# Kernel tuning notes

Measured on AMD Instinct MI355X. Metric: run time of the kernel, lower is better.

The kernel has to match this reference:

```python
import jax, jax.numpy as jnp
import numpy as np

TEMP_UPDATE = 1e-05
EPS = 1e-12  # torch F.normalize eps


def _l2norm(x, axis):
    n = jnp.sqrt(jnp.sum(x * x, axis=axis, keepdims=True))
    return x / jnp.maximum(n, EPS)


def setup_inputs() -> dict:
    key = jax.random.key(0)
    k1, k2 = jax.random.split(key)
    query = jax.random.normal(k1, (64, 256, 512), dtype=jnp.float32)
    keys = jax.random.normal(k2, (2048, 512), dtype=jnp.float32)
    return {"query": query, "keys": keys}


def reference(query, keys):
    bs, t, d = query.shape
    m = keys.shape[0]
    # F.normalize(query, dim=2)
    q = _l2norm(query, axis=2)
    qr = q.reshape(bs * t, d)                      # [N, d]
    score = qr @ keys.T                            # [N, m]
    score_query = jax.nn.softmax(score, axis=0)    # softmax over queries per slot
    score_memory = jax.nn.softmax(score, axis=1)   # softmax over slots per query
    # topk(1) over memory dim -> argmax slot per query
    g = jnp.argmax(score_memory, axis=1)           # [N] int
    col_max = jnp.max(score_query, axis=0)         # [m]
    # weight per query: score_query[n, g_n] / max(score_query[:, g_n])
    w = jnp.take_along_axis(score_query, g[:, None], axis=1)[:, 0] / col_max[g]
    # fused scatter-add replacing the per-slot python loop
    query_update = jax.ops.segment_sum(w[:, None] * qr, g, num_segments=m)  # [m, d]
    updated = _l2norm(TEMP_UPDATE * query_update + keys, axis=1)
    return jax.lax.stop_gradient(updated)  # original returns .detach()
```

## Files before the change

kernel.cpp:

```cpp
#include <hip/hip_runtime.h>
#include <math.h>

#define N_Q     16384
#define DDIM    512
#define M_SLOTS 2048
#define EPSN    1e-12f
#define TEMPU   1e-5f
#define KSCALE  25.4f
#define QSCALE  127.0f
#define INV_S   (1.0f / (127.0f * 25.4f))
#define NZBLK   73
#define BCAP    32

typedef unsigned int u32;
typedef unsigned long long u64;
typedef __attribute__((ext_vector_type(4))) int i32x4;

__device__ __forceinline__ void gld_lds16(const void* g, void* l) {
    __builtin_amdgcn_global_load_lds(
        (const __attribute__((address_space(1))) u32*)(g),
        (__attribute__((address_space(3))) u32*)(l), 16, 0, 0);
}
__device__ __forceinline__ float block_reduce_sum_128(float v, float* sred, int t) {
    #pragma unroll
    for (int o = 32; o > 0; o >>= 1) v += __shfl_down(v, o, 64);
    if ((t & 63) == 0) sred[t >> 6] = v;
    __syncthreads();
    return sred[0] + sred[1];
}
__device__ __forceinline__ char q8(float x, float s) {
    int v = __float2int_rn(x * s);
    v = v < -127 ? -127 : (v > 127 ? 127 : v);
    return (char)v;
}

__global__ __launch_bounds__(128) void k_prep(const float* __restrict__ q,
                                              const float* __restrict__ keys,
                                              char* __restrict__ qi8,
                                              char* __restrict__ ki8,
                                              float4* __restrict__ zbase) {
    __shared__ float sred[2];
    int b = blockIdx.x;
    int t = threadIdx.x;
    if (b < N_Q) {
        float4 v = ((const float4*)(q + (size_t)b * DDIM))[t];
        float ss = v.x * v.x + v.y * v.y + v.z * v.z + v.w * v.w;
        ss = block_reduce_sum_128(ss, sred, t);
        float s = QSCALE / fmaxf(sqrtf(ss), EPSN);
        char4 o;
        o.x = q8(v.x, s);
        o.y = q8(v.y, s);
        o.z = q8(v.z, s);
        o.w = q8(v.w, s);
        ((char4*)(qi8 + (size_t)b * DDIM))[t] = o;
    } else if (b < N_Q + M_SLOTS) {
        int r = b - N_Q;
        float4 v = ((const float4*)(keys + (size_t)r * DDIM))[t];
        char4 o;
        o.x = q8(v.x, KSCALE);
        o.y = q8(v.y, KSCALE);
        o.z = q8(v.z, KSCALE);
        o.w = q8(v.w, KSCALE);
        ((char4*)(ki8 + (size_t)r * DDIM))[t] = o;
    } else {
        int idx = (b - (N_Q + M_SLOTS)) * 128 + t;
        zbase[idx] = make_float4(0.f, 0.f, 0.f, 0.f);
    }
}

__global__ __launch_bounds__(256) void k_score(const char* __restrict__ qi8,
                                               const char* __restrict__ ki8,
                                               u64* __restrict__ rowpack,
                                               u32* __restrict__ colmax) {
    __shared__ char sA[3][128 * 64];
    __shared__ char sB[3][128 * 64];

    int t = threadIdx.x;
    int lane = t & 63;
    int wid = t >> 6;
    int wrow = wid >> 1;
    int wcol = wid & 1;
    int lr = lane & 15;
    int kc = lane >> 4;

    int n0 = blockIdx.y * 128;
    int j0 = blockIdx.x * 128;

    int srow = t >> 2;
    int scolB = (t & 3) * 16;

    const char* gA0 = qi8 + (size_t)(n0 + srow) * DDIM + scolB;
    const char* gA1 = qi8 + (size_t)(n0 + 64 + srow) * DDIM + scolB;
    const char* gB0 = ki8 + (size_t)(j0 + srow) * DDIM + scolB;
    const char* gB1 = ki8 + (size_t)(j0 + 64 + srow) * DDIM + scolB;

    i32x4 acc[4][4] = {};

#define STAGE(buf, k0)  do {                                   \
        gld_lds16(gA0 + (k0), &sA[buf][t * 16]);               \
        gld_lds16(gA1 + (k0), &sA[buf][4096 + t * 16]);        \
        gld_lds16(gB0 + (k0), &sB[buf][t * 16]);               \
        gld_lds16(gB1 + (k0), &sB[buf][4096 + t * 16]);        \
    } while (0)

    STAGE(0, 0);
    STAGE(1, 64);
    asm volatile("s_waitcnt vmcnt(4)" ::: "memory");
    __builtin_amdgcn_s_barrier();
    __builtin_amdgcn_sched_barrier(0);

    #pragma unroll
    for (int kt = 0; kt < 8; ++kt) {
        const int cur = kt % 3;
        if (kt < 6) STAGE((kt + 2) % 3, (kt + 2) * 64);

        i32x4 a[4], b[4];
        #pragma unroll
        for (int i = 0; i < 4; ++i)
            a[i] = *(const i32x4*)&sA[cur][(wrow * 64 + i * 16 + lr) * 64 + kc * 16];
        #pragma unroll
        for (int j = 0; j < 4; ++j)
            b[j] = *(const i32x4*)&sB[cur][(wcol * 64 + j * 16 + lr) * 64 + kc * 16];
        #pragma unroll
        for (int i = 0; i < 4; ++i)
            #pragma unroll
            for (int j = 0; j < 4; ++j)
                acc[i][j] = __builtin_amdgcn_mfma_i32_16x16x64_i8(a[i], b[j], acc[i][j], 0, 0, 0);

        if (kt < 6)       asm volatile("s_waitcnt vmcnt(4)" ::: "memory");
        else if (kt == 6) asm volatile("s_waitcnt vmcnt(0)" ::: "memory");
        if (kt < 7) {
            __builtin_amdgcn_s_barrier();
            __builtin_amdgcn_sched_barrier(0);
        }
    }
#undef STAGE

    #pragma unroll
    for (int i = 0; i < 4; ++i) {
        #pragma unroll
        for (int r = 0; r < 4; ++r) {
            int v = acc[i][0][r];
            int c = j0 + wcol * 64 + lr;
            #pragma unroll
            for (int j = 1; j < 4; ++j) {
                int vj = acc[i][j][r];
                int cj = j0 + wcol * 64 + j * 16 + lr;
                if (vj > v) { v = vj; c = cj; }
            }
            #pragma unroll
            for (int off = 1; off < 16; off <<= 1) {
                int ov = __shfl_xor(v, off, 64);
                int oc = __shfl_xor(c, off, 64);
                if (ov > v || (ov == v && oc < c)) { v = ov; c = oc; }
            }
            if (lr == 0) {
                int grow = n0 + wrow * 64 + i * 16 + kc * 4 + r;
                u64 pk = ((u64)(u32)(v ^ 0x80000000) << 32) | (u64)(~(u32)c);
                atomicMax(rowpack + grow, pk);
            }
        }
    }
    #pragma unroll
    for (int j = 0; j < 4; ++j) {
        int m = acc[0][j][0];
        #pragma unroll
        for (int i = 0; i < 4; ++i)
            #pragma unroll
            for (int r = 0; r < 4; ++r) m = max(m, acc[i][j][r]);
        m = max(m, __shfl_xor(m, 16, 64));
        m = max(m, __shfl_xor(m, 32, 64));
        if (kc == 0) atomicMax(colmax + j0 + wcol * 64 + j * 16 + lr,
                               (u32)m ^ 0x80000000u);
    }
}

__global__ __launch_bounds__(256) void k_fill(const u64* __restrict__ rowpack,
                                              const u32* __restrict__ colmax,
                                              u32* __restrict__ cur,
                                              u32* __restrict__ bperm,
                                              float* __restrict__ bw,
                                              u32* __restrict__ ovf_cnt,
                                              u32* __restrict__ ovf_n,
                                              float* __restrict__ ovf_w) {
    int n = blockIdx.x * 256 + threadIdx.x;
    u64 p = rowpack[n];
    int vi = (int)(((u32)(p >> 32)) ^ 0x80000000u);
    int g = (int)(~(u32)(p & 0xFFFFFFFFull));
    int cm = (int)(colmax[g] ^ 0x80000000u);
    float w = expf((float)(vi - cm) * INV_S);
    u32 pos = atomicAdd(cur + g, 1u);
    if (pos < BCAP) {
        bperm[g * BCAP + pos] = (u32)n;
        bw[g * BCAP + pos] = w;
    } else {
        u32 o = atomicAdd(ovf_cnt, 1u);
        ovf_n[o] = ((u32)g << 16) | (u32)n;
        ovf_w[o] = w;
    }
}

__global__ __launch_bounds__(128) void k_gather_final(const char* __restrict__ qi8,
                                                      const u32* __restrict__ cur,
                                                      const u32* __restrict__ bperm,
                                                      const float* __restrict__ bw,
                                                      const u32* __restrict__ ovf_cnt,
                                                      const u32* __restrict__ ovf_n,
                                                      const float* __restrict__ ovf_w,
                                                      const float* __restrict__ keys,
                                                      float* __restrict__ out) {
    __shared__ float sred[2];
    int j = blockIdx.x;
    int t = threadIdx.x;
    u32 c = cur[j];
    u32 cnt = c < BCAP ? c : BCAP;
    float ax = 0.f, ay = 0.f, az = 0.f, aw = 0.f;
    for (u32 i = 0; i < cnt; ++i) {
        u32 n = bperm[j * BCAP + i];
        float wq = bw[j * BCAP + i] * (1.0f / 127.0f);
        char4 q4 = ((const char4*)(qi8 + (size_t)n * DDIM))[t];
        ax = fmaf(wq, (float)q4.x, ax);
        ay = fmaf(wq, (float)q4.y, ay);
        az = fmaf(wq, (float)q4.z, az);
        aw = fmaf(wq, (float)q4.w, aw);
    }
    if (c > BCAP) {
        u32 oc = *ovf_cnt;
        for (u32 i = 0; i < oc; ++i) {
            u32 e = ovf_n[i];
            if ((e >> 16) == (u32)j) {
                u32 n = e & 0xFFFFu;
                float wq = ovf_w[i] * (1.0f / 127.0f);
                char4 q4 = ((const char4*)(qi8 + (size_t)n * DDIM))[t];
                ax = fmaf(wq, (float)q4.x, ax);
                ay = fmaf(wq, (float)q4.y, ay);
                az = fmaf(wq, (float)q4.z, az);
                aw = fmaf(wq, (float)q4.w, aw);
            }
        }
    }
    float4 k4 = ((const float4*)(keys + (size_t)j * DDIM))[t];
    float4 v;
    v.x = fmaf(TEMPU, ax, k4.x);
    v.y = fmaf(TEMPU, ay, k4.y);
    v.z = fmaf(TEMPU, az, k4.z);
    v.w = fmaf(TEMPU, aw, k4.w);
    float ss = v.x * v.x + v.y * v.y + v.z * v.z + v.w * v.w;
    ss = block_reduce_sum_128(ss, sred, t);
    float inv = 1.0f / fmaxf(sqrtf(ss), EPSN);
    v.x *= inv; v.y *= inv; v.z *= inv; v.w *= inv;
    ((float4*)(out + (size_t)j * DDIM))[t] = v;
}

extern "C" void kernel_launch(void* const* d_in, const int* in_sizes, int n_in,
                              void* d_out, int out_size, void* d_ws, size_t ws_size,
                              hipStream_t stream) {
    const float* query = (const float*)d_in[0];
    const float* keys  = (const float*)d_in[1];
    float* out = (float*)d_out;

    char* ws = (char*)d_ws;
    const size_t OFF_QI8   = 0;
    const size_t OFF_ROW   = 8388608;
    const size_t OFF_CMAX  = OFF_ROW + 131072;
    const size_t OFF_CUR   = OFF_CMAX + 8192;
    const size_t OFF_OVFC  = OFF_CUR + 8192;
    const size_t OFF_BPERM = OFF_OVFC + 2048;
    const size_t OFF_BW    = OFF_BPERM + 262144;
    const size_t OFF_OVFN  = OFF_BW + 262144;
    const size_t OFF_OVFW  = OFF_OVFN + 65536;
    const size_t OFF_KI8   = OFF_OVFW + 65536;

    char*   qi8    = ws + OFF_QI8;
    u64*    rowpack= (u64*)(ws + OFF_ROW);
    u32*    cmax   = (u32*)(ws + OFF_CMAX);
    u32*    cur    = (u32*)(ws + OFF_CUR);
    u32*    ovfc   = (u32*)(ws + OFF_OVFC);
    u32*    bperm  = (u32*)(ws + OFF_BPERM);
    float*  bw     = (float*)(ws + OFF_BW);
    u32*    ovfn   = (u32*)(ws + OFF_OVFN);
    float*  ovfw   = (float*)(ws + OFF_OVFW);
    char*   ki8    = ws + OFF_KI8;

    k_prep<<<N_Q + M_SLOTS + NZBLK, 128, 0, stream>>>(query, keys, qi8, ki8,
                                                      (float4*)(ws + OFF_ROW));

    dim3 g2(M_SLOTS / 128, N_Q / 128);
    k_score<<<g2, 256, 0, stream>>>(qi8, ki8, rowpack, cmax);

    k_fill<<<N_Q / 256, 256, 0, stream>>>(rowpack, cmax, cur, bperm, bw,
                                          ovfc, ovfn, ovfw);
    k_gather_final<<<M_SLOTS, 128, 0, stream>>>(qi8, cur, bperm, bw,
                                                ovfc, ovfn, ovfw, keys, out);
}
```

Before: 72.19 us.

## Make score GEMM persistent with cross-tile prefetch of next tile's K stages

Converts the int8 score GEMM from one block per 128x128 tile (2048 blocks) into a persistent grid of 768 blocks that stride over tiles. The triple-buffered global-to-LDS pipeline now continues across tile boundaries, so the first two K stages of the next tile load while the current tile's last stages compute and its argmax/colmax epilogue runs. This targets per-block launch and pipeline ramp-up cost, in exchange for uneven tile counts per block (2048/768 is not integral, so some blocks do 3 tiles and others 2) and more complex buffer indexing.

New measurement: 89.42 us. +23.9%, slower.

```diff
diff --git a/kernel.cpp b/kernel.cpp
--- a/kernel.cpp
+++ b/kernel.cpp
@@ -11,6 +11,7 @@
 #define INV_S   (1.0f / (127.0f * 25.4f))
 #define NZBLK   73
 #define BCAP    32
+#define PBLK    768
 
 typedef unsigned int u32;
 typedef unsigned long long u64;
@@ -83,96 +84,129 @@
     int lr = lane & 15;
     int kc = lane >> 4;
 
-    int n0 = blockIdx.y * 128;
-    int j0 = blockIdx.x * 128;
-
     int srow = t >> 2;
     int scolB = (t & 3) * 16;
 
-    const char* gA0 = qi8 + (size_t)(n0 + srow) * DDIM + scolB;
-    const char* gA1 = qi8 + (size_t)(n0 + 64 + srow) * DDIM + scolB;
-    const char* gB0 = ki8 + (size_t)(j0 + srow) * DDIM + scolB;
-    const char* gB1 = ki8 + (size_t)(j0 + 64 + srow) * DDIM + scolB;
+    int bid = blockIdx.x;
+    int nt = (2048 - bid + PBLK - 1) / PBLK;
+    int total = nt * 8;
+
+#define TILE_PTRS(tile, pA, pB)  do {                                  \
+        int n0_ = ((tile) >> 4) * 128;                                 \
+        int j0_ = ((tile) & 15) * 128;                                 \
+        pA = qi8 + (size_t)(n0_ + srow) * DDIM + scolB;                \
+        pB = ki8 + (size_t)(j0_ + srow) * DDIM + scolB;                \
+    } while (0)
+
+#define STAGE4(buf, pA, pB, koff)  do {                                \
+        gld_lds16((pA) + (koff),              &sA[buf][t * 16]);       \
+        gld_lds16((pA) + 64 * DDIM + (koff),  &sA[buf][4096 + t * 16]);\
+        gld_lds16((pB) + (koff),              &sB[buf][t * 16]);       \
+        gld_lds16((pB) + 64 * DDIM + (koff),  &sB[buf][4096 + t * 16]);\
+    } while (0)
 
     i32x4 acc[4][4] = {};
 
-#define STAGE(buf, k0)  do {                                   \
-        gld_lds16(gA0 + (k0), &sA[buf][t * 16]);               \
-        gld_lds16(gA1 + (k0), &sA[buf][4096 + t * 16]);        \
-        gld_lds16(gB0 + (k0), &sB[buf][t * 16]);               \
-        gld_lds16(gB1 + (k0), &sB[buf][4096 + t * 16]);        \
-    } while (0)
-
-    STAGE(0, 0);
-    STAGE(1, 64);
+    {
+        const char *pA, *pB;
+        TILE_PTRS(bid, pA, pB);
+        STAGE4(0, pA, pB, 0);
+        STAGE4(1, pA, pB, 64);
+    }
     asm volatile("s_waitcnt vmcnt(4)" ::: "memory");
     __builtin_amdgcn_s_barrier();
     __builtin_amdgcn_sched_barrier(0);
 
-    #pragma unroll
-    for (int kt = 0; kt < 8; ++kt) {
-        const int cur = kt % 3;
-        if (kt < 6) STAGE((kt + 2) % 3, (kt + 2) * 64);
-
-        i32x4 a[4], b[4];
+    int b0 = 0;
+    #pragma unroll 1
+    for (int tt = 0; tt < nt; ++tt) {
+        int tileC = bid + tt * PBLK;
+        int n0 = (tileC >> 4) * 128;
+        int j0 = (tileC & 15) * 128;
+        int tileN = (tt + 1 < nt) ? tileC + PBLK : tileC;
+        const char *cA, *cB, *nA, *nB;
+        TILE_PTRS(tileC, cA, cB);
+        TILE_PTRS(tileN, nA, nB);
+        int bufs[3] = { b0, (b0 + 1) % 3, (b0 + 2) % 3 };
+
         #pragma unroll
-        for (int i = 0; i < 4; ++i)
-            a[i] = *(const i32x4*)&sA[cur][(wrow * 64 + i * 16 + lr) * 64 + kc * 16];
+        for (int kt = 0; kt < 8; ++kt) {
+            int vs = tt * 8 + kt;
+            if (vs + 2 < total) {
+                int sbuf = bufs[(kt + 2) % 3];
+                if (kt < 6) STAGE4(sbuf, cA, cB, (kt + 2) * 64);
+                else        STAGE4(sbuf, nA, nB, (kt - 6) * 64);
+            }
+            {
+                int cbuf = bufs[kt % 3];
+                i32x4 a[4], b[4];
+                #pragma unroll
+                for (int i = 0; i < 4; ++i)
+                    a[i] = *(const i32x4*)&sA[cbuf][(wrow * 64 + i * 16 + lr) * 64 + kc * 16];
+                #pragma unroll
+                for (int j = 0; j < 4; ++j)
+                    b[j] = *(const i32x4*)&sB[cbuf][(wcol * 64 + j * 16 + lr) * 64 + kc * 16];
+                #pragma unroll
+                for (int i = 0; i < 4; ++i)
+                    #pragma unroll
+                    for (int j = 0; j < 4; ++j)
+                        acc[i][j] = __builtin_amdgcn_mfma_i32_16x16x64_i8(a[i], b[j], acc[i][j], 0, 0, 0);
+            }
+            if (vs + 2 < total)       asm volatile("s_waitcnt vmcnt(4)" ::: "memory");
+            else if (vs == total - 2) asm volatile("s_waitcnt vmcnt(0)" ::: "memory");
+            if (vs < total - 1) {
+                __builtin_amdgcn_s_barrier();
+                __builtin_amdgcn_sched_barrier(0);
+            }
+        }
+
         #pragma unroll
-        for (int j = 0; j < 4; ++j)
-            b[j] = *(const i32x4*)&sB[cur][(wcol * 64 + j * 16 + lr) * 64 + kc * 16];
+        for (int i = 0; i < 4; ++i) {
+            #pragma unroll
+            for (int r = 0; r < 4; ++r) {
+                int v = acc[i][0][r];
+                int c = j0 + wcol * 64 + lr;
+                #pragma unroll
+                for (int j = 1; j < 4; ++j) {
+                    int vj = acc[i][j][r];
+                    int cj = j0 + wcol * 64 + j * 16 + lr;
+                    if (vj > v) { v = vj; c = cj; }
+                }
+                #pragma unroll
+                for (int off = 1; off < 16; off <<= 1) {
+                    int ov = __shfl_xor(v, off, 64);
+                    int oc = __shfl_xor(c, off, 64);
+                    if (ov > v || (ov == v && oc < c)) { v = ov; c = oc; }
+                }
+                if (lr == 0) {
+                    int grow = n0 + wrow * 64 + i * 16 + kc * 4 + r;
+                    u64 pk = ((u64)(u32)(v ^ 0x80000000) << 32) | (u64)(~(u32)c);
+                    atomicMax(rowpack + grow, pk);
+                }
+            }
+        }
+        #pragma unroll
+        for (int j = 0; j < 4; ++j) {
+            int m = acc[0][j][0];
+            #pragma unroll
+            for (int i = 0; i < 4; ++i)
+                #pragma unroll
+                for (int r = 0; r < 4; ++r) m = max(m, acc[i][j][r]);
+            m = max(m, __shfl_xor(m, 16, 64));
+            m = max(m, __shfl_xor(m, 32, 64));
+            if (kc == 0) atomicMax(colmax + j0 + wcol * 64 + j * 16 + lr,
+                                   (u32)m ^ 0x80000000u);
+        }
         #pragma unroll
         for (int i = 0; i < 4; ++i)
             #pragma unroll
             for (int j = 0; j < 4; ++j)
-                acc[i][j] = __builtin_amdgcn_mfma_i32_16x16x64_i8(a[i], b[j], acc[i][j], 0, 0, 0);
-
-        if (kt < 6)       asm volatile("s_waitcnt vmcnt(4)" ::: "memory");
-        else if (kt == 6) asm volatile("s_waitcnt vmcnt(0)" ::: "memory");
-        if (kt < 7) {
-            __builtin_amdgcn_s_barrier();
-            __builtin_amdgcn_sched_barrier(0);
-        }
-    }
-#undef STAGE
-
-    #pragma unroll
-    for (int i = 0; i < 4; ++i) {
-        #pragma unroll
-        for (int r = 0; r < 4; ++r) {
-            int v = acc[i][0][r];
-            int c = j0 + wcol * 64 + lr;
-            #pragma unroll
-            for (int j = 1; j < 4; ++j) {
-                int vj = acc[i][j][r];
-                int cj = j0 + wcol * 64 + j * 16 + lr;
-                if (vj > v) { v = vj; c = cj; }
-            }
-            #pragma unroll
-            for (int off = 1; off < 16; off <<= 1) {
-                int ov = __shfl_xor(v, off, 64);
-                int oc = __shfl_xor(c, off, 64);
-                if (ov > v || (ov == v && oc < c)) { v = ov; c = oc; }
-            }
-            if (lr == 0) {
-                int grow = n0 + wrow * 64 + i * 16 + kc * 4 + r;
-                u64 pk = ((u64)(u32)(v ^ 0x80000000) << 32) | (u64)(~(u32)c);
-                atomicMax(rowpack + grow, pk);
-            }
-        }
-    }
-    #pragma unroll
-    for (int j = 0; j < 4; ++j) {
-        int m = acc[0][j][0];
-        #pragma unroll
-        for (int i = 0; i < 4; ++i)
-            #pragma unroll
-            for (int r = 0; r < 4; ++r) m = max(m, acc[i][j][r]);
-        m = max(m, __shfl_xor(m, 16, 64));
-        m = max(m, __shfl_xor(m, 32, 64));
-        if (kc == 0) atomicMax(colmax + j0 + wcol * 64 + j * 16 + lr,
-                               (u32)m ^ 0x80000000u);
-    }
+                acc[i][j] = (i32x4){0, 0, 0, 0};
+
+        b0 = (b0 + 2) % 3;
+    }
+#undef STAGE4
+#undef TILE_PTRS
 }
 
 __global__ __launch_bounds__(256) void k_fill(const u64* __restrict__ rowpack,
@@ -285,8 +319,7 @@
     k_prep<<<N_Q + M_SLOTS + NZBLK, 128, 0, stream>>>(query, keys, qi8, ki8,
                                                       (float4*)(ws + OFF_ROW));
 
-    dim3 g2(M_SLOTS / 128, N_Q / 128);
-    k_score<<<g2, 256, 0, stream>>>(qi8, ki8, rowpack, cmax);
+    k_score<<<PBLK, 256, 0, stream>>>(qi8, ki8, rowpack, cmax);
 
     k_fill<<<N_Q / 256, 256, 0, stream>>>(rowpack, cmax, cur, bperm, bw,
                                           ovfc, ovfn, ovfw);
```

## Restructure int8 score GEMM: full-K key tile in swizzled LDS, query fragments in registers

Applied to the files above, without the earlier changes.

The score kernel now handles a 128x64 output tile per block instead of 128x128. Each block loads the entire 64x512 key tile into LDS once, with an XOR swizzle to avoid bank conflicts. Each wave loads its 32 query rows for the full K dimension straight from global memory into registers, which removes the triple-buffered K pipeline and its per-step barriers. In exchange, the grid has twice as many blocks, each query row is fetched once per 64 keys instead of once per 128, more registers are held, and the global loads are no longer overlapped with compute.

Measured after the change: 78.14 us. 8.2% more time.

```diff
diff --git a/kernel.cpp b/kernel.cpp
--- a/kernel.cpp
+++ b/kernel.cpp
@@ -72,80 +72,67 @@
                                                const char* __restrict__ ki8,
                                                u64* __restrict__ rowpack,
                                                u32* __restrict__ colmax) {
-    __shared__ char sA[3][128 * 64];
-    __shared__ char sB[3][128 * 64];
+    __shared__ char sB[64 * 512];
 
     int t = threadIdx.x;
     int lane = t & 63;
-    int wid = t >> 6;
-    int wrow = wid >> 1;
-    int wcol = wid & 1;
+    int w = t >> 6;
     int lr = lane & 15;
     int kc = lane >> 4;
 
+    int j0 = blockIdx.x * 64;
     int n0 = blockIdx.y * 128;
-    int j0 = blockIdx.x * 128;
-
-    int srow = t >> 2;
-    int scolB = (t & 3) * 16;
-
-    const char* gA0 = qi8 + (size_t)(n0 + srow) * DDIM + scolB;
-    const char* gA1 = qi8 + (size_t)(n0 + 64 + srow) * DDIM + scolB;
-    const char* gB0 = ki8 + (size_t)(j0 + srow) * DDIM + scolB;
-    const char* gB1 = ki8 + (size_t)(j0 + 64 + srow) * DDIM + scolB;
-
-    i32x4 acc[4][4] = {};
-
-#define STAGE(buf, k0)  do {                                   \
-        gld_lds16(gA0 + (k0), &sA[buf][t * 16]);               \
-        gld_lds16(gA1 + (k0), &sA[buf][4096 + t * 16]);        \
-        gld_lds16(gB0 + (k0), &sB[buf][t * 16]);               \
-        gld_lds16(gB1 + (k0), &sB[buf][4096 + t * 16]);        \
-    } while (0)
-
-    STAGE(0, 0);
-    STAGE(1, 64);
-    asm volatile("s_waitcnt vmcnt(4)" ::: "memory");
-    __builtin_amdgcn_s_barrier();
-    __builtin_amdgcn_sched_barrier(0);
-
+    int wr0 = n0 + w * 32;
+
+    #pragma unroll
+    for (int i = 0; i < 8; ++i) {
+        int m = i * 256 + t;
+        int row = m >> 5;
+        int slot = m & 31;
+        int gcol = (slot * 16) ^ ((row & 15) << 4);
+        gld_lds16(ki8 + (size_t)(j0 + row) * DDIM + gcol, &sB[m * 16]);
+    }
+
+    const char* ga0 = qi8 + (size_t)(wr0 + lr) * DDIM + kc * 16;
+    const char* ga1 = qi8 + (size_t)(wr0 + 16 + lr) * DDIM + kc * 16;
+    i32x4 a[8][2];
     #pragma unroll
     for (int kt = 0; kt < 8; ++kt) {
-        const int cur = kt % 3;
-        if (kt < 6) STAGE((kt + 2) % 3, (kt + 2) * 64);
-
-        i32x4 a[4], b[4];
-        #pragma unroll
-        for (int i = 0; i < 4; ++i)
-            a[i] = *(const i32x4*)&sA[cur][(wrow * 64 + i * 16 + lr) * 64 + kc * 16];
-        #pragma unroll
-        for (int j = 0; j < 4; ++j)
-            b[j] = *(const i32x4*)&sB[cur][(wcol * 64 + j * 16 + lr) * 64 + kc * 16];
-        #pragma unroll
-        for (int i = 0; i < 4; ++i)
-            #pragma unroll
-            for (int j = 0; j < 4; ++j)
-                acc[i][j] = __builtin_amdgcn_mfma_i32_16x16x64_i8(a[i], b[j], acc[i][j], 0, 0, 0);
-
-        if (kt < 6)       asm volatile("s_waitcnt vmcnt(4)" ::: "memory");
-        else if (kt == 6) asm volatile("s_waitcnt vmcnt(0)" ::: "memory");
-        if (kt < 7) {
-            __builtin_amdgcn_s_barrier();
-            __builtin_amdgcn_sched_barrier(0);
-        }
-    }
-#undef STAGE
-
-    #pragma unroll
-    for (int i = 0; i < 4; ++i) {
+        a[kt][0] = *(const i32x4*)(ga0 + kt * 64);
+        a[kt][1] = *(const i32x4*)(ga1 + kt * 64);
+    }
+    #pragma unroll
+    for (int kt = 0; kt < 8; ++kt)
+        asm volatile("" :: "v"(a[kt][0]), "v"(a[kt][1]));
+
+    asm volatile("s_waitcnt vmcnt(0)" ::: "memory");
+    __syncthreads();
+
+    i32x4 acc[2][4] = {};
+    #pragma unroll
+    for (int kt = 0; kt < 8; ++kt) {
+        i32x4 b[4];
+        #pragma unroll
+        for (int jj = 0; jj < 4; ++jj)
+            b[jj] = *(const i32x4*)&sB[(jj * 16 + lr) * 512 +
+                                       ((kt * 64 + kc * 16) ^ (lr << 4))];
+        #pragma unroll
+        for (int i = 0; i < 2; ++i)
+            #pragma unroll
+            for (int jj = 0; jj < 4; ++jj)
+                acc[i][jj] = __builtin_amdgcn_mfma_i32_16x16x64_i8(a[kt][i], b[jj], acc[i][jj], 0, 0, 0);
+    }
+
+    #pragma unroll
+    for (int i = 0; i < 2; ++i) {
         #pragma unroll
         for (int r = 0; r < 4; ++r) {
             int v = acc[i][0][r];
-            int c = j0 + wcol * 64 + lr;
-            #pragma unroll
-            for (int j = 1; j < 4; ++j) {
-                int vj = acc[i][j][r];
-                int cj = j0 + wcol * 64 + j * 16 + lr;
+            int c = j0 + lr;
+            #pragma unroll
+            for (int jj = 1; jj < 4; ++jj) {
+                int vj = acc[i][jj][r];
+                int cj = j0 + jj * 16 + lr;
                 if (vj > v) { v = vj; c = cj; }
             }
             #pragma unroll
@@ -155,22 +142,22 @@
                 if (ov > v || (ov == v && oc < c)) { v = ov; c = oc; }
             }
             if (lr == 0) {
-                int grow = n0 + wrow * 64 + i * 16 + kc * 4 + r;
+                int grow = wr0 + i * 16 + kc * 4 + r;
                 u64 pk = ((u64)(u32)(v ^ 0x80000000) << 32) | (u64)(~(u32)c);
                 atomicMax(rowpack + grow, pk);
             }
         }
     }
     #pragma unroll
-    for (int j = 0; j < 4; ++j) {
-        int m = acc[0][j][0];
-        #pragma unroll
-        for (int i = 0; i < 4; ++i)
-            #pragma unroll
-            for (int r = 0; r < 4; ++r) m = max(m, acc[i][j][r]);
+    for (int jj = 0; jj < 4; ++jj) {
+        int m = acc[0][jj][0];
+        #pragma unroll
+        for (int i = 0; i < 2; ++i)
+            #pragma unroll
+            for (int r = 0; r < 4; ++r) m = max(m, acc[i][jj][r]);
         m = max(m, __shfl_xor(m, 16, 64));
         m = max(m, __shfl_xor(m, 32, 64));
-        if (kc == 0) atomicMax(colmax + j0 + wcol * 64 + j * 16 + lr,
+        if (kc == 0) atomicMax(colmax + j0 + jj * 16 + lr,
                                (u32)m ^ 0x80000000u);
     }
 }
@@ -285,7 +272,7 @@
     k_prep<<<N_Q + M_SLOTS + NZBLK, 128, 0, stream>>>(query, keys, qi8, ki8,
                                                       (float4*)(ws + OFF_ROW));
 
-    dim3 g2(M_SLOTS / 128, N_Q / 128);
+    dim3 g2(M_SLOTS / 64, N_Q / 128);
     k_score<<<g2, 256, 0, stream>>>(qi8, ki8, rowpack, cmax);
 
     k_fill<<<N_Q / 256, 256, 0, stream>>>(rowpack, cmax, cur, bperm, bw,
```

## Enlarge int8 score GEMM tile to 256x256 with 8 waves and swizzled LDS

Applied to the files above, without the earlier changes.

The score kernel moves from 128x128 tiles with 4 waves to 256x256 tiles with 8 waves. Each wave now computes a 128x64 sub-tile with 8x4 accumulators, which raises arithmetic intensity and cuts global loads per MFMA. Staging becomes double-buffered, with the next A/B chunks issued inside the MFMA sub-steps. An XOR swizzle on the LDS columns is meant to avoid bank conflicts, and s_setprio is raised around the MFMA bursts. The trade-offs are more accumulator registers, more barriers per k-step, and only 512 blocks, which may lower occupancy or CU balance.

New measurement: 79.55 us. 1.1x slower.

```diff
diff --git a/kernel.cpp b/kernel.cpp
--- a/kernel.cpp
+++ b/kernel.cpp
@@ -68,84 +68,96 @@
     }
 }
 
-__global__ __launch_bounds__(256) void k_score(const char* __restrict__ qi8,
+__global__ __launch_bounds__(512) void k_score(const char* __restrict__ qi8,
                                                const char* __restrict__ ki8,
                                                u64* __restrict__ rowpack,
                                                u32* __restrict__ colmax) {
-    __shared__ char sA[3][128 * 64];
-    __shared__ char sB[3][128 * 64];
+    __shared__ char sA[2][2][128 * 64];
+    __shared__ char sB[2][2][128 * 64];
 
     int t = threadIdx.x;
     int lane = t & 63;
     int wid = t >> 6;
-    int wrow = wid >> 1;
-    int wcol = wid & 1;
+    int wr = wid >> 2;
+    int wc = wid & 3;
     int lr = lane & 15;
     int kc = lane >> 4;
 
-    int n0 = blockIdx.y * 128;
-    int j0 = blockIdx.x * 128;
+    int j0 = blockIdx.x * 256;
+    int n0 = blockIdx.y * 256;
 
     int srow = t >> 2;
-    int scolB = (t & 3) * 16;
-
-    const char* gA0 = qi8 + (size_t)(n0 + srow) * DDIM + scolB;
-    const char* gA1 = qi8 + (size_t)(n0 + 64 + srow) * DDIM + scolB;
-    const char* gB0 = ki8 + (size_t)(j0 + srow) * DDIM + scolB;
-    const char* gB1 = ki8 + (size_t)(j0 + 64 + srow) * DDIM + scolB;
-
-    i32x4 acc[4][4] = {};
-
-#define STAGE(buf, k0)  do {                                   \
-        gld_lds16(gA0 + (k0), &sA[buf][t * 16]);               \
-        gld_lds16(gA1 + (k0), &sA[buf][4096 + t * 16]);        \
-        gld_lds16(gB0 + (k0), &sB[buf][t * 16]);               \
-        gld_lds16(gB1 + (k0), &sB[buf][4096 + t * 16]);        \
-    } while (0)
-
-    STAGE(0, 0);
-    STAGE(1, 64);
-    asm volatile("s_waitcnt vmcnt(4)" ::: "memory");
+    int gcol = 16 * ((t & 3) ^ ((t >> 3) & 3));
+    int roff = 16 * (kc ^ ((lr >> 1) & 3));
+
+    const char* baseA = qi8 + (size_t)(n0 + srow) * DDIM + gcol;
+    const char* baseB = ki8 + (size_t)(j0 + srow) * DDIM + gcol;
+
+#define SA(tt, h) gld_lds16(baseA + (size_t)(h) * 128 * DDIM + (tt) * 64, \
+                            &sA[(tt) & 1][h][t * 16])
+#define SB(tt, h) gld_lds16(baseB + (size_t)(h) * 128 * DDIM + (tt) * 64, \
+                            &sB[(tt) & 1][h][t * 16])
+
+    i32x4 acc[8][4] = {};
+    i32x4 b[4];
+
+    SA(0, 0); SA(0, 1); SB(0, 0); SB(0, 1); SB(1, 0); SB(1, 1);
+    asm volatile("s_waitcnt vmcnt(2)" ::: "memory");
     __builtin_amdgcn_s_barrier();
     __builtin_amdgcn_sched_barrier(0);
 
     #pragma unroll
-    for (int kt = 0; kt < 8; ++kt) {
-        const int cur = kt % 3;
-        if (kt < 6) STAGE((kt + 2) % 3, (kt + 2) * 64);
-
-        i32x4 a[4], b[4];
+    for (int tt = 0; tt < 8; ++tt) {
+        const int buf = tt & 1;
         #pragma unroll
-        for (int i = 0; i < 4; ++i)
-            a[i] = *(const i32x4*)&sA[cur][(wrow * 64 + i * 16 + lr) * 64 + kc * 16];
-        #pragma unroll
-        for (int j = 0; j < 4; ++j)
-            b[j] = *(const i32x4*)&sB[cur][(wcol * 64 + j * 16 + lr) * 64 + kc * 16];
-        #pragma unroll
-        for (int i = 0; i < 4; ++i)
+        for (int p = 0; p < 4; ++p) {
+            if (p == 0) {
+                #pragma unroll
+                for (int j = 0; j < 4; ++j)
+                    b[j] = *(const i32x4*)&sB[buf][wc >> 1]
+                               [((wc & 1) * 64 + j * 16 + lr) * 64 + roff];
+            }
+            i32x4 a0 = *(const i32x4*)&sA[buf][wr][((2 * p) * 16 + lr) * 64 + roff];
+            i32x4 a1 = *(const i32x4*)&sA[buf][wr][((2 * p + 1) * 16 + lr) * 64 + roff];
+            if      (p == 0) { if (tt < 7) SA(tt + 1, 0); }
+            else if (p == 1) { if (tt < 7) SA(tt + 1, 1); }
+            else if (p == 2) { if (tt < 6) SB(tt + 2, 0); }
+            else             { if (tt < 6) SB(tt + 2, 1); }
+            __builtin_amdgcn_s_barrier();
+            asm volatile("s_waitcnt lgkmcnt(0)" ::: "memory");
+            __builtin_amdgcn_sched_barrier(0);
+            __builtin_amdgcn_s_setprio(1);
             #pragma unroll
-            for (int j = 0; j < 4; ++j)
-                acc[i][j] = __builtin_amdgcn_mfma_i32_16x16x64_i8(a[i], b[j], acc[i][j], 0, 0, 0);
-
-        if (kt < 6)       asm volatile("s_waitcnt vmcnt(4)" ::: "memory");
-        else if (kt == 6) asm volatile("s_waitcnt vmcnt(0)" ::: "memory");
-        if (kt < 7) {
-            __builtin_amdgcn_s_barrier();
-            __builtin_amdgcn_sched_barrier(0);
+            for (int j = 0; j < 4; ++j) {
+                acc[2 * p][j] =
+                    __builtin_amdgcn_mfma_i32_16x16x64_i8(a0, b[j], acc[2 * p][j], 0, 0, 0);
+                acc[2 * p + 1][j] =
+                    __builtin_amdgcn_mfma_i32_16x16x64_i8(a1, b[j], acc[2 * p + 1][j], 0, 0, 0);
+            }
+            __builtin_amdgcn_s_setprio(0);
+            if (p == 3) {
+                if (tt < 6)       asm volatile("s_waitcnt vmcnt(2)" ::: "memory");
+                else if (tt == 6) asm volatile("s_waitcnt vmcnt(0)" ::: "memory");
+            }
+            if (!(tt == 7 && p == 3)) {
+                __builtin_amdgcn_s_barrier();
+                __builtin_amdgcn_sched_barrier(0);
+            }
         }
     }
-#undef STAGE
+#undef SA
+#undef SB
 
     #pragma unroll
-    for (int i = 0; i < 4; ++i) {
+    for (int f = 0; f < 8; ++f) {
         #pragma unroll
         for (int r = 0; r < 4; ++r) {
-            int v = acc[i][0][r];
-            int c = j0 + wcol * 64 + lr;
+            int v = acc[f][0][r];
+            int c = j0 + wc * 64 + lr;
             #pragma unroll
             for (int j = 1; j < 4; ++j) {
-                int vj = acc[i][j][r];
-                int cj = j0 + wcol * 64 + j * 16 + lr;
+                int vj = acc[f][j][r];
+                int cj = j0 + wc * 64 + j * 16 + lr;
                 if (vj > v) { v = vj; c = cj; }
             }
             #pragma unroll
@@ -155,7 +167,7 @@
                 if (ov > v || (ov == v && oc < c)) { v = ov; c = oc; }
             }
             if (lr == 0) {
-                int grow = n0 + wrow * 64 + i * 16 + kc * 4 + r;
+                int grow = n0 + wr * 128 + f * 16 + kc * 4 + r;
                 u64 pk = ((u64)(u32)(v ^ 0x80000000) << 32) | (u64)(~(u32)c);
                 atomicMax(rowpack + grow, pk);
             }
@@ -165,12 +177,12 @@
     for (int j = 0; j < 4; ++j) {
         int m = acc[0][j][0];
         #pragma unroll
-        for (int i = 0; i < 4; ++i)
+        for (int f = 0; f < 8; ++f)
             #pragma unroll
-            for (int r = 0; r < 4; ++r) m = max(m, acc[i][j][r]);
+            for (int r = 0; r < 4; ++r) m = max(m, acc[f][j][r]);
         m = max(m, __shfl_xor(m, 16, 64));
         m = max(m, __shfl_xor(m, 32, 64));
-        if (kc == 0) atomicMax(colmax + j0 + wcol * 64 + j * 16 + lr,
+        if (kc == 0) atomicMax(colmax + j0 + wc * 64 + j * 16 + lr,
                                (u32)m ^ 0x80000000u);
     }
 }
@@ -285,8 +297,8 @@
     k_prep<<<N_Q + M_SLOTS + NZBLK, 128, 0, stream>>>(query, keys, qi8, ki8,
                                                       (float4*)(ws + OFF_ROW));
 
-    dim3 g2(M_SLOTS / 128, N_Q / 128);
-    k_score<<<g2, 256, 0, stream>>>(qi8, ki8, rowpack, cmax);
+    dim3 g2(M_SLOTS / 256, N_Q / 256);
+    k_score<<<g2, 512, 0, stream>>>(qi8, ki8, rowpack, cmax);
 
     k_fill<<<N_Q / 256, 256, 0, stream>>>(rowpack, cmax, cur, bperm, bw,
                                           ovfc, ovfn, ovfw);
```
